# Kernel optimization log

Measured on AMD Instinct MI355X. Metric: run time of the kernel, lower is better.

Reference implementation:

```python
import jax, jax.numpy as jnp
import numpy as np

# TT-linear: in_features=1024 -> out_features=4096
IN_DIMS = (8, 8, 4, 4)      # m1..m4, prod = 1024
OUT_DIMS = (8, 8, 8, 8)     # n1..n4, prod = 4096
RANKS = (1, 16, 16, 16, 1)  # r0..r4
IN_FEATURES = 1024
OUT_FEATURES = 4096
BATCH, SEQ = 4, 1024


def _init_core(key, shape):
    # uniform(-1,1)/sqrt(fan_in-ish), matching the original's uniform-style init scale
    fan = shape[0] * shape[1]
    return (2.0 * jax.random.uniform(key, shape, dtype=jnp.float32) - 1.0) / np.sqrt(fan).astype(np.float32)


def setup_inputs() -> dict:
    key = jax.random.key(0)
    ks = jax.random.split(key, 6)
    x = jax.random.normal(ks[0], (BATCH, SEQ, IN_FEATURES), dtype=jnp.float32)
    core0 = _init_core(ks[1], (1, 8, 8, 16))    # [r0, m1, n1, r1]
    core1 = _init_core(ks[2], (16, 8, 8, 16))   # [r1, m2, n2, r2]
    core2 = _init_core(ks[3], (16, 4, 8, 16))   # [r2, m3, n3, r3]
    core3 = _init_core(ks[4], (16, 4, 8, 1))    # [r3, m4, n4, r4]
    bias = (2.0 * jax.random.uniform(ks[5], (OUT_FEATURES,), dtype=jnp.float32) - 1.0) / np.sqrt(OUT_FEATURES).astype(np.float32)
    return {"x": x, "core0": core0, "core1": core1, "core2": core2, "core3": core3, "bias": bias}


def reference(x, core0, core1, core2, core3, bias):
    lead = x.shape[:-1]
    # split the feature axis into TT input factors: [T, m1, m2, m3, m4]
    t = x.reshape((-1,) + IN_DIMS)
    c0 = core0[0]        # [m1, n1, r1]   (boundary rank r0 = 1 squeezed)
    c3 = core3[..., 0]   # [r3, m4, n4]   (boundary rank r4 = 1 squeezed)
    # sequential TT core chain: absorb one m_k, emit one n_k per step
    t = jnp.einsum('tijkl,ixp->tjklxp', t, c0)      # [T, m2,m3,m4, n1, r1]
    t = jnp.einsum('tjklxp,pjyq->tklxyq', t, core1)  # [T, m3,m4, n1,n2, r2]
    t = jnp.einsum('tklxyq,qkzr->tlxyzr', t, core2)  # [T, m4, n1,n2,n3, r3]
    t = jnp.einsum('tlxyzr,rlw->txyzw', t, c3)       # [T, n1,n2,n3,n4]
    y = t.reshape(lead + (OUT_FEATURES,)) + bias
    return y
```

## Files before the change

kernel.cpp:

```cpp
#include <hip/hip_runtime.h>
#include <hip/hip_bf16.h>
#include <cstdint>


typedef __bf16 bf16x8 __attribute__((ext_vector_type(8)));
typedef float f32x4 __attribute__((ext_vector_type(4)));

__device__ __forceinline__ void g2lds16(const void* g, void* l) {
    __builtin_amdgcn_global_load_lds(
        (const __attribute__((address_space(1))) void*)g,
        (__attribute__((address_space(3))) void*)l,
        16, 0, 0);
}

__global__ __launch_bounds__(256) void prep(
    const float* __restrict__ x, __bf16* __restrict__ xb,
    const float* __restrict__ c0, const float* __restrict__ c1,
    const float* __restrict__ c2, const float* __restrict__ c3,
    __bf16* __restrict__ wt) {
    const int b = blockIdx.x;
    const int t = threadIdx.x;
    if (b < 2048) {
        const int i = (b * 256 + t) * 8;
        float4 a0 = *(const float4*)(x + i);
        float4 a1 = *(const float4*)(x + i + 4);
        bf16x8 o;
        o[0] = (__bf16)a0.x; o[1] = (__bf16)a0.y; o[2] = (__bf16)a0.z; o[3] = (__bf16)a0.w;
        o[4] = (__bf16)a1.x; o[5] = (__bf16)a1.y; o[6] = (__bf16)a1.z; o[7] = (__bf16)a1.w;
        *(bf16x8*)(xb + i) = o;
        return;
    }
    __shared__ float t12[4][16];
    __shared__ float t123[4][512];
    __shared__ float c3s[512];
    #pragma unroll
    for (int i = t; i < 512; i += 256) c3s[i] = c3[i];
    const int s = t >> 6;
    const int lane = t & 63;
    const int g = (b - 2048) * 4 + s;
    const int m1 = g >> 9, n1 = (g >> 6) & 7, m2 = (g >> 3) & 7, n2 = g & 7;
    __syncthreads();
    if (lane < 16) {
        const int r2 = lane;
        float sum = 0.f;
        #pragma unroll
        for (int r1 = 0; r1 < 16; ++r1)
            sum += c0[(m1 * 8 + n1) * 16 + r1] * c1[((r1 * 8 + m2) * 8 + n2) * 16 + r2];
        t12[s][r2] = sum;
    }
    __syncthreads();
    #pragma unroll
    for (int idx = lane; idx < 512; idx += 64) {
        const int m3 = idx >> 7, n3 = (idx >> 4) & 7, r3 = idx & 15;
        float sum = 0.f;
        #pragma unroll
        for (int r2 = 0; r2 < 16; ++r2)
            sum += t12[s][r2] * c2[((r2 * 4 + m3) * 8 + n3) * 16 + r3];
        t123[s][(m3 * 8 + n3) * 16 + r3] = sum;
    }
    __syncthreads();
    const int n3 = lane >> 3, n4 = lane & 7;
    const int n = ((n1 * 8 + n2) * 8 + n3) * 8 + n4;
    const int kbase = (m1 * 8 + m2) * 16;
    float v[16];
    #pragma unroll
    for (int e = 0; e < 16; ++e) v[e] = 0.f;
    #pragma unroll
    for (int m3 = 0; m3 < 4; ++m3) {
        #pragma unroll
        for (int r3 = 0; r3 < 16; ++r3) {
            const float tv = t123[s][(m3 * 8 + n3) * 16 + r3];
            #pragma unroll
            for (int m4 = 0; m4 < 4; ++m4)
                v[m3 * 4 + m4] += tv * c3s[(r3 * 4 + m4) * 8 + n4];
        }
    }
    bf16x8 lo, hi;
    #pragma unroll
    for (int e = 0; e < 8; ++e) { lo[e] = (__bf16)v[e]; hi[e] = (__bf16)v[8 + e]; }
    *(bf16x8*)(wt + (size_t)n * 1024 + kbase)     = lo;
    *(bf16x8*)(wt + (size_t)n * 1024 + kbase + 8) = hi;
}


#define SCHED() __builtin_amdgcn_sched_barrier(0)
#define BAR()  do { SCHED(); __builtin_amdgcn_s_barrier(); SCHED(); } while (0)
#define WAITVM(n) do { SCHED(); asm volatile("s_waitcnt vmcnt(" #n ")"); SCHED(); } while (0)

__global__ __launch_bounds__(512, 2) void tt_gemm(
    const __bf16* __restrict__ A, const __bf16* __restrict__ B,
    const float* __restrict__ bias, float* __restrict__ C) {
    constexpr int K = 1024, N = 4096;
    constexpr int NKT = 16;
    __shared__ __bf16 sA[2][2][256 * 32];
    __shared__ __bf16 sB[2][2][256 * 32];
    const int t = threadIdx.x;
    const int lane = t & 63;
    const int wave = t >> 6;
    const int wm = (wave >> 2) * 128;
    const int wn = (wave & 3) * 64;
    const int l15 = lane & 15, lh = lane >> 4;
    const int cOff = ((lh ^ ((l15 >> 1) & 3)) << 4);

    const int xcd = blockIdx.x & 7;
    const int lid = blockIdx.x >> 3;
    const int bm = ((xcd >> 2) * 8 + (lid & 7)) * 256;
    const int bn = ((xcd & 3) * 4 + (lid >> 3)) * 256;

    const int c0i = t, c1i = t + 512;
    const int r0 = c0i >> 2, r1 = c1i >> 2;
    const int lc0 = (c0i & 3) ^ ((r0 >> 1) & 3);
    const int lc1 = (c1i & 3) ^ ((r1 >> 1) & 3);
    const __bf16* a0p = A + (size_t)(bm + r0) * K + lc0 * 8;
    const __bf16* a1p = A + (size_t)(bm + r1) * K + lc1 * 8;
    const __bf16* b0p = B + (size_t)(bn + r0) * K + lc0 * 8;
    const __bf16* b1p = B + (size_t)(bn + r1) * K + lc1 * 8;

#define ST_A(kt, ks) do { \
    g2lds16(a0p + (size_t)(kt) * 64 + (ks) * 32, (char*)&sA[(kt) & 1][ks][0] + c0i * 16); \
    g2lds16(a1p + (size_t)(kt) * 64 + (ks) * 32, (char*)&sA[(kt) & 1][ks][0] + c1i * 16); } while (0)
#define ST_B(kt, ks) do { \
    g2lds16(b0p + (size_t)(kt) * 64 + (ks) * 32, (char*)&sB[(kt) & 1][ks][0] + c0i * 16); \
    g2lds16(b1p + (size_t)(kt) * 64 + (ks) * 32, (char*)&sB[(kt) & 1][ks][0] + c1i * 16); } while (0)
#define LDA(dst, fi, ks) dst = *(const bf16x8*)((const char*)&sA[slot][ks][0] + (wm + (fi) * 16 + l15) * 64 + cOff)
#define LDB(dst, ni, ks) dst = *(const bf16x8*)((const char*)&sB[slot][ks][0] + (wn + (ni) * 16 + l15) * 64 + cOff)
#define MFMA16(base, afr) do { \
    __builtin_amdgcn_s_setprio(1); \
    _Pragma("unroll") \
    for (int mi = 0; mi < 4; ++mi) \
        _Pragma("unroll") \
        for (int ni = 0; ni < 4; ++ni) \
            acc[(base) + mi][ni] = __builtin_amdgcn_mfma_f32_16x16x32_bf16( \
                afr[mi], bb[ni], acc[(base) + mi][ni], 0, 0, 0); \
    __builtin_amdgcn_s_setprio(0); } while (0)

    f32x4 acc[8][4] = {};

    ST_A(0, 0); ST_B(0, 0);
    ST_A(0, 1); ST_B(0, 1);
    ST_A(1, 0); ST_B(1, 0);
    WAITVM(4);
    BAR();

    #pragma unroll 1
    for (int kt = 0; kt < NKT; ++kt) {
        const int slot = kt & 1;
        bf16x8 aL[4], aH[4], bb[4];
        #pragma unroll
        for (int mi = 0; mi < 4; ++mi) LDA(aL[mi], mi, 0);
        #pragma unroll
        for (int ni = 0; ni < 4; ++ni) LDB(bb[ni], ni, 0);
        #pragma unroll
        for (int mi = 0; mi < 4; ++mi) LDA(aH[mi], 4 + mi, 0);
        if (kt < NKT - 1) { ST_A(kt + 1, 1); ST_B(kt + 1, 1); }
        MFMA16(0, aL);
        MFMA16(4, aH);
        BAR();
        #pragma unroll
        for (int mi = 0; mi < 4; ++mi) LDA(aL[mi], mi, 1);
        #pragma unroll
        for (int ni = 0; ni < 4; ++ni) LDB(bb[ni], ni, 1);
        #pragma unroll
        for (int mi = 0; mi < 4; ++mi) LDA(aH[mi], 4 + mi, 1);
        if (kt < NKT - 2) { ST_A(kt + 2, 0); ST_B(kt + 2, 0); }
        MFMA16(0, aL);
        MFMA16(4, aH);
        if (kt < NKT - 2)       { WAITVM(4); }
        else if (kt == NKT - 2) { WAITVM(0); }
        BAR();
    }

    float bv[4];
    #pragma unroll
    for (int ni = 0; ni < 4; ++ni) bv[ni] = bias[bn + wn + ni * 16 + l15];
    #pragma unroll
    for (int mi = 0; mi < 8; ++mi) {
        #pragma unroll
        for (int r = 0; r < 4; ++r) {
            const int row = bm + wm + mi * 16 + lh * 4 + r;
            float* crow = C + (size_t)row * N + bn + wn + l15;
            #pragma unroll
            for (int ni = 0; ni < 4; ++ni)
                crow[ni * 16] = acc[mi][ni][r] + bv[ni];
        }
    }
#undef ST_A
#undef ST_B
#undef LDA
#undef LDB
#undef MFMA16
}

extern "C" void kernel_launch(void* const* d_in, const int* in_sizes, int n_in,
                              void* d_out, int out_size, void* d_ws, size_t ws_size,
                              hipStream_t stream) {
    const float* x    = (const float*)d_in[0];
    const float* c0   = (const float*)d_in[1];
    const float* c1   = (const float*)d_in[2];
    const float* c2   = (const float*)d_in[3];
    const float* c3   = (const float*)d_in[4];
    const float* bias = (const float*)d_in[5];
    float* out = (float*)d_out;

    __bf16* xb = (__bf16*)d_ws;
    __bf16* wt = xb + (size_t)4096 * 1024;

    prep<<<3072, 256, 0, stream>>>(x, xb, c0, c1, c2, c3, wt);
    tt_gemm<<<256, 512, 0, stream>>>(xb, wt, bias, out);
}
```

Before: 134.7 us.

## Switch GEMM inner loop from 16x16x32 to 32x32x16 bf16 MFMA tiles

Replaces the 16x16x32 MFMA fragments with 32x32x16 MFMA, so each wave covers its 128x64 tile with 4x2 accumulators of 16 floats. This lowers LDS fragment reads per MFMA and the instruction count. The LDS reads are rescheduled across the barrier: most of the second k-half fragments are loaded before the first barrier, and only the high-k A fragments are loaded after it. The epilogue is rewritten for the 32x32 output layout. The trade-off is higher register pressure from the fragments held across the barrier, and the new swizzle and row mapping must be correct.

```diff
diff --git a/kernel.cpp b/kernel.cpp
--- a/kernel.cpp
+++ b/kernel.cpp
@@ -5,6 +5,7 @@
 
 typedef __bf16 bf16x8 __attribute__((ext_vector_type(8)));
 typedef float f32x4 __attribute__((ext_vector_type(4)));
+typedef float f32x16 __attribute__((ext_vector_type(16)));
 
 __device__ __forceinline__ void g2lds16(const void* g, void* l) {
     __builtin_amdgcn_global_load_lds(
@@ -99,8 +100,10 @@
     const int wave = t >> 6;
     const int wm = (wave >> 2) * 128;
     const int wn = (wave & 3) * 64;
-    const int l15 = lane & 15, lh = lane >> 4;
-    const int cOff = ((lh ^ ((l15 >> 1) & 3)) << 4);
+    const int l31 = lane & 31, lk = lane >> 5;
+    const int key = (l31 >> 1) & 3;
+    const int cO0 = ((0 * 2 + lk) ^ key) << 4;
+    const int cO1 = ((1 * 2 + lk) ^ key) << 4;
 
     const int xcd = blockIdx.x & 7;
     const int lid = blockIdx.x >> 3;
@@ -122,19 +125,23 @@
 #define ST_B(kt, ks) do { \
     g2lds16(b0p + (size_t)(kt) * 64 + (ks) * 32, (char*)&sB[(kt) & 1][ks][0] + c0i * 16); \
     g2lds16(b1p + (size_t)(kt) * 64 + (ks) * 32, (char*)&sB[(kt) & 1][ks][0] + c1i * 16); } while (0)
-#define LDA(dst, fi, ks) dst = *(const bf16x8*)((const char*)&sA[slot][ks][0] + (wm + (fi) * 16 + l15) * 64 + cOff)
-#define LDB(dst, ni, ks) dst = *(const bf16x8*)((const char*)&sB[slot][ks][0] + (wn + (ni) * 16 + l15) * 64 + cOff)
-#define MFMA16(base, afr) do { \
+#define LDA32(dst, mi, kk, ks) dst = *(const bf16x8*)((const char*)&sA[slot][ks][0] \
+    + (wm + (mi) * 32 + l31) * 64 + ((kk) ? cO1 : cO0))
+#define LDB32(dst, ni, kk, ks) dst = *(const bf16x8*)((const char*)&sB[slot][ks][0] \
+    + (wn + (ni) * 32 + l31) * 64 + ((kk) ? cO1 : cO0))
+#define MFMA_HALF(a, b) do { \
     __builtin_amdgcn_s_setprio(1); \
     _Pragma("unroll") \
-    for (int mi = 0; mi < 4; ++mi) \
+    for (int kk = 0; kk < 2; ++kk) \
         _Pragma("unroll") \
-        for (int ni = 0; ni < 4; ++ni) \
-            acc[(base) + mi][ni] = __builtin_amdgcn_mfma_f32_16x16x32_bf16( \
-                afr[mi], bb[ni], acc[(base) + mi][ni], 0, 0, 0); \
+        for (int mi = 0; mi < 4; ++mi) \
+            _Pragma("unroll") \
+            for (int ni = 0; ni < 2; ++ni) \
+                acc[mi][ni] = __builtin_amdgcn_mfma_f32_32x32x16_bf16( \
+                    a[mi][kk], b[ni][kk], acc[mi][ni], 0, 0, 0); \
     __builtin_amdgcn_s_setprio(0); } while (0)
 
-    f32x4 acc[8][4] = {};
+    f32x16 acc[4][2] = {};
 
     ST_A(0, 0); ST_B(0, 0);
     ST_A(0, 1); ST_B(0, 1);
@@ -145,50 +152,45 @@
     #pragma unroll 1
     for (int kt = 0; kt < NKT; ++kt) {
         const int slot = kt & 1;
-        bf16x8 aL[4], aH[4], bb[4];
-        #pragma unroll
-        for (int mi = 0; mi < 4; ++mi) LDA(aL[mi], mi, 0);
-        #pragma unroll
-        for (int ni = 0; ni < 4; ++ni) LDB(bb[ni], ni, 0);
-        #pragma unroll
-        for (int mi = 0; mi < 4; ++mi) LDA(aH[mi], 4 + mi, 0);
+        bf16x8 a0f[4][2], b0f[2][2], a1f[4][2], b1f[2][2];
+        #pragma unroll
+        for (int mi = 0; mi < 4; ++mi) { LDA32(a0f[mi][0], mi, 0, 0); LDA32(a0f[mi][1], mi, 1, 0); }
+        #pragma unroll
+        for (int ni = 0; ni < 2; ++ni) { LDB32(b0f[ni][0], ni, 0, 0); LDB32(b0f[ni][1], ni, 1, 0); }
+        #pragma unroll
+        for (int ni = 0; ni < 2; ++ni) { LDB32(b1f[ni][0], ni, 0, 1); LDB32(b1f[ni][1], ni, 1, 1); }
+        #pragma unroll
+        for (int mi = 0; mi < 4; ++mi) LDA32(a1f[mi][0], mi, 0, 1);
         if (kt < NKT - 1) { ST_A(kt + 1, 1); ST_B(kt + 1, 1); }
-        MFMA16(0, aL);
-        MFMA16(4, aH);
+        MFMA_HALF(a0f, b0f);
         BAR();
         #pragma unroll
-        for (int mi = 0; mi < 4; ++mi) LDA(aL[mi], mi, 1);
-        #pragma unroll
-        for (int ni = 0; ni < 4; ++ni) LDB(bb[ni], ni, 1);
-        #pragma unroll
-        for (int mi = 0; mi < 4; ++mi) LDA(aH[mi], 4 + mi, 1);
+        for (int mi = 0; mi < 4; ++mi) LDA32(a1f[mi][1], mi, 1, 1);
         if (kt < NKT - 2) { ST_A(kt + 2, 0); ST_B(kt + 2, 0); }
-        MFMA16(0, aL);
-        MFMA16(4, aH);
+        MFMA_HALF(a1f, b1f);
         if (kt < NKT - 2)       { WAITVM(4); }
         else if (kt == NKT - 2) { WAITVM(0); }
         BAR();
     }
 
-    float bv[4];
-    #pragma unroll
-    for (int ni = 0; ni < 4; ++ni) bv[ni] = bias[bn + wn + ni * 16 + l15];
-    #pragma unroll
-    for (int mi = 0; mi < 8; ++mi) {
-        #pragma unroll
-        for (int r = 0; r < 4; ++r) {
-            const int row = bm + wm + mi * 16 + lh * 4 + r;
-            float* crow = C + (size_t)row * N + bn + wn + l15;
-            #pragma unroll
-            for (int ni = 0; ni < 4; ++ni)
-                crow[ni * 16] = acc[mi][ni][r] + bv[ni];
+    float bv[2];
+    #pragma unroll
+    for (int ni = 0; ni < 2; ++ni) bv[ni] = bias[bn + wn + ni * 32 + l31];
+    #pragma unroll
+    for (int mi = 0; mi < 4; ++mi) {
+        #pragma unroll
+        for (int r = 0; r < 16; ++r) {
+            const int row = bm + wm + mi * 32 + (r & 3) + 8 * (r >> 2) + 4 * lk;
+            float* crow = C + (size_t)row * N + bn + wn + l31;
+            crow[0]  = acc[mi][0][r] + bv[0];
+            crow[32] = acc[mi][1][r] + bv[1];
         }
     }
 #undef ST_A
 #undef ST_B
-#undef LDA
-#undef LDB
-#undef MFMA16
+#undef LDA32
+#undef LDB32
+#undef MFMA_HALF
 }
 
 extern "C" void kernel_launch(void* const* d_in, const int* in_sizes, int n_in,
```

Result: slower. 138.9 us (+3.2%).
